# Kernel tuning notes

Measured on AMD Instinct MI355X. Metric: run time of the kernel, lower is better.

The kernel has to match this reference:

```python
import jax, jax.numpy as jnp
import numpy as np

B, C, H, W = 4, 128, 64, 64

def setup_inputs() -> dict:
    key = jax.random.key(0)
    ks = jax.random.split(key, 4)
    X = jax.random.normal(ks[0], (B, C, H, W), dtype=jnp.float32)
    Wq = jax.random.normal(ks[1], (C, C), dtype=jnp.float32) * 0.05
    Wk = jax.random.normal(ks[2], (C, C), dtype=jnp.float32) * 0.05
    Wv = jax.random.normal(ks[3], (C, C), dtype=jnp.float32) * 0.05
    bq = jnp.zeros((C,), dtype=jnp.float32)
    bk = jnp.zeros((C,), dtype=jnp.float32)
    bv = jnp.zeros((C,), dtype=jnp.float32)
    return {"X": X, "Wq": Wq, "bq": bq, "Wk": Wk, "bk": bk, "Wv": Wv, "bv": bv}

def reference(X, Wq, bq, Wk, bk, Wv, bv):
    b, c, h, w = X.shape
    hw = h * w
    # 1x1 conv == per-pixel linear over channels
    def proj(Wm, bias):
        y = jnp.einsum('bchw,oc->bohw', X, Wm) + bias[None, :, None, None]
        return y.reshape(b, c, hw).transpose(0, 2, 1)  # (b, hw, c)
    q = proj(Wq, bq)
    k = proj(Wk, bk)
    v = proj(Wv, bv)
    scores = jnp.einsum('bic,bjc->bij', q, k)  # (b, hw_q, hw_k); no 1/sqrt(d)
    # torch Softmax(dim=1) on (b, hw, hw): normalize over the QUERY axis
    a = jax.nn.softmax(scores, axis=1)
    x = jnp.einsum('bij,bjc->bic', a, v)  # (b, hw, c)
    x = x.transpose(0, 2, 1).reshape(b, c, h, w)
    return X + x
```

## Files before the change

### kernel.cpp

```cpp
#include <hip/hip_runtime.h>
#include <hip/hip_bf16.h>


typedef unsigned short u16;
typedef __attribute__((ext_vector_type(8))) __bf16 bf16x8;
typedef __attribute__((ext_vector_type(8))) unsigned short us8;
typedef __attribute__((ext_vector_type(4))) float f32x4;
typedef __attribute__((ext_vector_type(16))) float f32x16;

#define NB 4
#define CH 128
#define NP 4096
#define JSPL 4
#define ISPL 8

__device__ __forceinline__ float bf2f(u16 b){ union{float f;unsigned u;}v; v.u=((unsigned)b)<<16; return v.f; }
__device__ __forceinline__ u16 f2bf(float f){ union{float f;unsigned u;}v; v.f=f; unsigned r=v.u + 0x7FFFu + ((v.u>>16)&1u); return (u16)(r>>16); }

__device__ __forceinline__ f32x4 mfma16(bf16x8 a, bf16x8 b, f32x4 c){
  return __builtin_amdgcn_mfma_f32_16x16x32_bf16(a, b, c, 0, 0, 0);
}
__device__ __forceinline__ f32x16 mfma32(bf16x8 a, bf16x8 b, f32x16 c){
  return __builtin_amdgcn_mfma_f32_32x32x16_bf16(a, b, c, 0, 0, 0);
}
__device__ __forceinline__ bf16x8 ld8(const u16* p){
  union { us8 u; bf16x8 b; } v; v.u = *(const us8*)p; return v.b;
}
__device__ __forceinline__ void split8(const float* p, bf16x8& h, bf16x8& l){
  union { us8 u; bf16x8 b; } uh, ul;
  #pragma unroll
  for (int e=0;e<8;++e){
    float f = p[e];
    u16 hb = f2bf(f);
    uh.u[e] = hb;
    ul.u[e] = f2bf(f - bf2f(hb));
  }
  h = uh.b; l = ul.b;
}
__device__ __forceinline__ unsigned pk2(float a, float b){
  float2 f2; f2.x = a; f2.y = b;
  __hip_bfloat162 hb = __float22bfloat162_rn(f2);
  unsigned u; __builtin_memcpy(&u, &hb, 4);
  return u;
}
__device__ __forceinline__ void gll16(const void* g, void* l){
  __builtin_amdgcn_global_load_lds((const __attribute__((address_space(1))) void*)g,
                                   (__attribute__((address_space(3))) void*)l, 16, 0, 0);
}

__global__ __launch_bounds__(256) void wsplit_kernel(
    const float* __restrict__ Wq, const float* __restrict__ Wk,
    const float* __restrict__ Wv, u16* __restrict__ Whi, u16* __restrict__ Wlo)
{
  const int m = blockIdx.y;
  const float* W = (m==0) ? Wq : (m==1) ? Wk : Wv;
  int i = blockIdx.x*256 + threadIdx.x;
  float f = W[i];
  u16 hb = f2bf(f);
  Whi[m*CH*CH + i] = hb;
  Wlo[m*CH*CH + i] = f2bf(f - bf2f(hb));
}

__global__ __launch_bounds__(64) void proj_kernel(
    const float* __restrict__ X,
    const u16* __restrict__ Whi, const u16* __restrict__ Wlo,
    const float* __restrict__ bq, const float* __restrict__ bk,
    const float* __restrict__ bv,
    u16* __restrict__ Qhi, u16* __restrict__ Qlo,
    u16* __restrict__ Khi, u16* __restrict__ Klo,
    u16* __restrict__ Vthi, u16* __restrict__ Vtlo)
{
  __shared__ float XT[16][CH+4];
  const int b = blockIdx.y, p0 = blockIdx.x*16, lane = threadIdx.x;
  #pragma unroll
  for (int h=0; h<2; ++h){
    int c = lane + h*64;
    const float* src = X + ((size_t)b*CH + c)*NP + p0;
    #pragma unroll
    for (int v4=0; v4<4; ++v4){
      f32x4 v = *(const f32x4*)(src + v4*4);
      #pragma unroll
      for (int p=0;p<4;++p) XT[v4*4+p][c] = v[p];
    }
  }
  __syncthreads();
  const int l15 = lane&15, quad = lane>>4;
  bf16x8 xh[4], xl[4];
  #pragma unroll
  for (int s=0;s<4;++s) split8(&XT[l15][s*32+quad*8], xh[s], xl[s]);

  const float* bm[2] = {bq, bk};
  u16* OH[2] = {Qhi, Khi};
  u16* OL[2] = {Qlo, Klo};
  #pragma unroll
  for (int m=0;m<2;++m){
    const u16* WH = Whi + m*CH*CH;
    const u16* WL = Wlo + m*CH*CH;
    #pragma unroll
    for (int nt=0;nt<8;++nt){
      f32x4 a = {0.f,0.f,0.f,0.f};
      #pragma unroll
      for (int s=0;s<4;++s){
        size_t g = (size_t)(nt*16+l15)*CH + s*32 + quad*8;
        bf16x8 wh = ld8(&WH[g]), wl = ld8(&WL[g]);
        a = mfma16(xh[s], wl, a);
        a = mfma16(xl[s], wh, a);
        a = mfma16(xh[s], wh, a);
      }
      int o = nt*16 + l15;
      float bias = bm[m][o];
      #pragma unroll
      for (int r=0;r<4;++r){
        int i = p0 + quad*4 + r;
        float q = a[r] + bias;
        u16 hb = f2bf(q);
        size_t idx = ((size_t)b*NP + i)*CH + o;
        OH[m][idx] = hb;
        OL[m][idx] = f2bf(q - bf2f(hb));
      }
    }
  }
  const u16* WH = Whi + 2*CH*CH;
  const u16* WL = Wlo + 2*CH*CH;
  #pragma unroll
  for (int mt=0;mt<8;++mt){
    f32x4 a = {0.f,0.f,0.f,0.f};
    #pragma unroll
    for (int s=0;s<4;++s){
      size_t g = (size_t)(mt*16+l15)*CH + s*32 + quad*8;
      bf16x8 wh = ld8(&WH[g]), wl = ld8(&WL[g]);
      a = mfma16(wh, xl[s], a);
      a = mfma16(wl, xh[s], a);
      a = mfma16(wh, xh[s], a);
    }
    #pragma unroll
    for (int r=0;r<4;++r){
      int co = mt*16 + quad*4 + r;
      float v = a[r] + bv[co];
      u16 hb = f2bf(v);
      size_t idx = ((size_t)b*CH + co)*NP + p0 + l15;
      Vthi[idx] = hb;
      Vtlo[idx] = f2bf(v - bf2f(hb));
    }
  }
}

__global__ __launch_bounds__(256,3) void stats_kernel(
    const u16* __restrict__ Qhi, const u16* __restrict__ Qlo,
    const u16* __restrict__ Khi, const u16* __restrict__ Klo,
    float* __restrict__ colpart)
{
  __shared__ u16 SQ[2][2][32*CH];
  const int b = blockIdx.z, isplit = blockIdx.y;
  const int tid = threadIdx.x, lane = tid&63, w = tid>>6;
  const int l31 = lane&31, h = lane>>5;
  const int j0w = blockIdx.x*128 + w*32;

  const int slot0 = w*128 + lane, slot1 = slot0 + 64;
  const int qr0 = slot0&31, qc0 = slot0>>5, qr1 = slot1&31, qc1 = slot1>>5;
  const size_t qg0 = ((size_t)b*NP + qr0)*CH + qc0*8;
  const size_t qg1 = ((size_t)b*NP + qr1)*CH + qc1*8;
  const int lof0 = slot0*8, lof1 = slot1*8;

  bf16x8 kh[8], kl[8];
  #pragma unroll
  for (int ks=0;ks<8;++ks){
    size_t g = ((size_t)b*NP + j0w + l31)*CH + ks*16 + h*8;
    kh[ks] = ld8(&Khi[g]);
    kl[ks] = ld8(&Klo[g]);
  }

  const int ibase = isplit*(NP/ISPL);
  const int NCH = (NP/ISPL)/32;

  auto stageQ = [&](int t){
    size_t iofs = (size_t)(ibase + t*32)*CH;
    int bf = t&1;
    gll16(&Qhi[qg0 + iofs], &SQ[bf][0][lof0]);
    gll16(&Qhi[qg1 + iofs], &SQ[bf][0][lof1]);
    gll16(&Qlo[qg0 + iofs], &SQ[bf][1][lof0]);
    gll16(&Qlo[qg1 + iofs], &SQ[bf][1][lof1]);
  };
  auto computeS = [&](int t, f32x16& s){
    const u16* Qh = &SQ[t&1][0][0];
    const u16* Ql = &SQ[t&1][1][0];
    #pragma unroll
    for (int r=0;r<16;++r) s[r] = 0.f;
    #pragma unroll
    for (int ks=0;ks<8;++ks){
      int o = (ks*2+h)*256 + l31*8;
      bf16x8 qbh = ld8(&Qh[o]);
      bf16x8 qbl = ld8(&Ql[o]);
      s = mfma32(kh[ks], qbl, s);
      s = mfma32(kl[ks], qbh, s);
      s = mfma32(kh[ks], qbh, s);
    }
  };

  stageQ(0); stageQ(1);
  __syncthreads();
  f32x16 s;
  computeS(0, s);
  __syncthreads();

  float scol[16];
  #pragma unroll
  for (int r=0;r<16;++r) scol[r] = 0.f;

  for (int ic=0; ic<NCH; ++ic){
    if (ic+2 < NCH) stageQ(ic+2);
    #pragma unroll
    for (int r=0;r<16;++r) scol[r] += __expf(s[r]);
    if (ic+1 < NCH) computeS(ic+1, s);
    __syncthreads();
  }
  #pragma unroll
  for (int m=1; m<32; m<<=1){
    #pragma unroll
    for (int r=0;r<16;++r) scol[r] += __shfl_xor(scol[r], m);
  }
  if (l31 == 0){
    #pragma unroll
    for (int r=0;r<16;++r){
      int j = j0w + (r&3) + 8*(r>>2) + 4*h;
      colpart[((size_t)(isplit*NB + b))*NP + j] = scol[r];
    }
  }
}

__global__ __launch_bounds__(256) void scalev_kernel(
    u16* __restrict__ Vthi, const u16* __restrict__ Vtlo,
    const float* __restrict__ colpart)
{
  size_t t = (size_t)blockIdx.x*256 + threadIdx.x;
  size_t base = t*8;
  int bc = (int)(base >> 12);
  int b  = bc >> 7;
  int j0 = (int)(base & (NP-1));
  f32x4 s0 = {0.f,0.f,0.f,0.f}, s1 = {0.f,0.f,0.f,0.f};
  #pragma unroll
  for (int k=0;k<ISPL;++k){
    const float* cp = &colpart[((size_t)(k*NB + b))*NP + j0];
    f32x4 a0 = *(const f32x4*)cp;
    f32x4 a1 = *(const f32x4*)(cp+4);
    #pragma unroll
    for (int e=0;e<4;++e){ s0[e]+=a0[e]; s1[e]+=a1[e]; }
  }
  us8 hh = *(const us8*)&Vthi[base];
  us8 ll = *(const us8*)&Vtlo[base];
  us8 oh;
  #pragma unroll
  for (int e=0;e<8;++e){
    float r = 1.0f / (e<4 ? s0[e] : s1[e-4]);
    float v = (bf2f(hh[e]) + bf2f(ll[e])) * r;
    oh[e] = f2bf(v);
  }
  *(us8*)&Vthi[base] = oh;
}

__global__ __launch_bounds__(256) void copyx_kernel(
    const float* __restrict__ X, float* __restrict__ out)
{
  size_t idx = ((size_t)blockIdx.x*256 + threadIdx.x)*4;
  *(f32x4*)&out[idx] = *(const f32x4*)&X[idx];
}

__global__ __launch_bounds__(256,2) void attn_kernel(
    const u16* __restrict__ Qhi, const u16* __restrict__ Qlo,
    const u16* __restrict__ Khi, const u16* __restrict__ Klo,
    const u16* __restrict__ Vthi,
    float* __restrict__ out)
{
  __shared__ u16 SK[2][2][32*CH];
  __shared__ u16 SV[2][4*CH*8];
  const int b = blockIdx.z, jsplit = blockIdx.y;
  const int tid = threadIdx.x, lane = tid&63, w = tid>>6;
  const int l31 = lane&31, h = lane>>5;
  const int i0w = blockIdx.x*128 + w*32;
  const bool hb1 = (h != 0);

  const int slot0 = tid, slot1 = tid + 256;
  const int kr0 = slot0&31, kc0 = slot0>>5, kr1 = slot1&31, kc1 = slot1>>5;
  const int vr0 = slot0&127, vc0 = slot0>>7, vr1 = slot1&127, vc1 = slot1>>7;
  const size_t kg0 = ((size_t)b*NP + kr0)*CH + kc0*8;
  const size_t kg1 = ((size_t)b*NP + kr1)*CH + kc1*8;
  const size_t vg0 = ((size_t)b*CH + vr0)*NP + vc0*8;
  const size_t vg1 = ((size_t)b*CH + vr1)*NP + vc1*8;
  const int lof0 = slot0*8, lof1 = slot1*8;

  const int jbase = jsplit*(NP/JSPL);
  const int NJT = (NP/JSPL)/32;

  auto stageK = [&](int t){
    size_t jofs = (size_t)(jbase + t*32)*CH;
    int bf = t&1;
    gll16(&Khi[kg0 + jofs], &SK[bf][0][lof0]);
    gll16(&Khi[kg1 + jofs], &SK[bf][0][lof1]);
    gll16(&Klo[kg0 + jofs], &SK[bf][1][lof0]);
    gll16(&Klo[kg1 + jofs], &SK[bf][1][lof1]);
  };
  auto stageV = [&](int t){
    int j0 = jbase + t*32;
    int bf = t&1;
    gll16(&Vthi[vg0 + j0], &SV[bf][lof0]);
    gll16(&Vthi[vg1 + j0], &SV[bf][lof1]);
  };

  bf16x8 qh[8], ql[8];
  #pragma unroll
  for (int ks=0;ks<8;++ks){
    size_t g = ((size_t)b*NP + i0w + l31)*CH + ks*16 + h*8;
    qh[ks] = ld8(&Qhi[g]); ql[ks] = ld8(&Qlo[g]);
  }

  auto computeS = [&](int t, f32x16& s){
    const u16* Kh = &SK[t&1][0][0];
    const u16* Kl = &SK[t&1][1][0];
    #pragma unroll
    for (int r=0;r<16;++r) s[r] = 0.f;
    #pragma unroll
    for (int ks=0;ks<8;++ks){
      int o = (ks*2+h)*256 + l31*8;
      bf16x8 ah = ld8(&Kh[o]);
      bf16x8 al = ld8(&Kl[o]);
      s = mfma32(ah, ql[ks], s);
      s = mfma32(al, qh[ks], s);
      s = mfma32(ah, qh[ks], s);
    }
  };

  f32x16 acc[4];
  #pragma unroll
  for (int mt=0;mt<4;++mt)
    #pragma unroll
    for (int r=0;r<16;++r) acc[mt][r] = 0.f;

  stageK(0); stageV(0); stageK(1);
  __syncthreads();
  f32x16 s;
  computeS(0, s);
  __syncthreads();

  for (int jt=0; jt<NJT; ++jt){
    const int cb = jt&1;
    if (jt+2 < NJT) stageK(jt+2);
    if (jt+1 < NJT) stageV(jt+1);

    float p[16];
    #pragma unroll
    for (int r=0;r<16;++r) p[r] = __expf(s[r]);

    if (jt+1 < NJT) computeS(jt+1, s);

    const u16* Vh = &SV[cb][0];
    #pragma unroll
    for (int t=0;t<2;++t){
      unsigned hA = pk2(p[8*t+0], p[8*t+1]);
      unsigned hB = pk2(p[8*t+2], p[8*t+3]);
      unsigned hC = pk2(p[8*t+4], p[8*t+5]);
      unsigned hD = pk2(p[8*t+6], p[8*t+7]);
      unsigned s0h = hb1? hA:hC, s1h = hb1? hB:hD;
      unsigned r0h = __shfl_xor(s0h, 32), r1h = __shfl_xor(s1h, 32);
      unsigned dh[4];
      dh[0] = hb1? r0h : hA;  dh[1] = hb1? r1h : hB;
      dh[2] = hb1? hC  : r0h; dh[3] = hb1? hD  : r1h;
      bf16x8 Bh;
      __builtin_memcpy(&Bh, dh, 16);
      #pragma unroll
      for (int mt=0;mt<4;++mt){
        int o = (t*2+h)*1024 + (mt*32+l31)*8;
        bf16x8 vh = ld8(&Vh[o]);
        acc[mt] = mfma32(vh, Bh, acc[mt]);
      }
    }
    __syncthreads();
  }
  float* xp = out + (size_t)b*CH*NP;
  #pragma unroll
  for (int mt=0;mt<4;++mt){
    #pragma unroll
    for (int r=0;r<16;++r){
      int c = mt*32 + (r&3) + 8*(r>>2) + 4*h;
      atomicAdd(&xp[(size_t)c*NP + i0w + l31], acc[mt][r]);
    }
  }
}

extern "C" void kernel_launch(void* const* d_in, const int* in_sizes, int n_in,
                              void* d_out, int out_size, void* d_ws, size_t ws_size,
                              hipStream_t stream)
{
  const float* X  = (const float*)d_in[0];
  const float* Wq = (const float*)d_in[1];
  const float* bq = (const float*)d_in[2];
  const float* Wk = (const float*)d_in[3];
  const float* bk = (const float*)d_in[4];
  const float* Wv = (const float*)d_in[5];
  const float* bv = (const float*)d_in[6];
  float* outp = (float*)d_out;

  const size_t n = (size_t)NB*NP*CH;
  u16* Qhi = (u16*)d_ws;
  u16* Qlo = Qhi + n;
  u16* Khi = Qlo + n;
  u16* Klo = Khi + n;
  u16* Vthi = Klo + n;
  u16* Vtlo = Vthi + n;
  u16* Whi  = Vtlo + n;
  u16* Wlo  = Whi + 3*CH*CH;
  float* colpart = (float*)(Wlo + 3*CH*CH);

  wsplit_kernel<<<dim3(CH*CH/256, 3),      256, 0, stream>>>(Wq, Wk, Wv, Whi, Wlo);
  proj_kernel  <<<dim3(NP/16, NB),          64, 0, stream>>>(X, Whi, Wlo, bq, bk, bv,
                                                             Qhi,Qlo, Khi,Klo, Vthi,Vtlo);
  stats_kernel <<<dim3(NP/128, ISPL, NB),  256, 0, stream>>>(Qhi,Qlo, Khi,Klo, colpart);
  scalev_kernel<<<dim3(n/(256*8)),         256, 0, stream>>>(Vthi, Vtlo, colpart);
  copyx_kernel <<<dim3(n/(256*4)),         256, 0, stream>>>(X, outp);
  attn_kernel  <<<dim3(NP/128, JSPL, NB),  256, 0, stream>>>(Qhi,Qlo, Khi,Klo,
                                                             Vthi, outp);
}
```

Before: 254.4 us.

## Materialize exp scores in stats pass and reuse them in attention

The stats kernel now writes the bf16 exp(S) matrix, already packed in MFMA fragment order, to a workspace buffer. A new attention kernel then streams P and V from memory instead of recomputing QK^T with three split-precision MFMAs per tile. This trades the second score computation for writing and reading a 4x4096x4096 bf16 buffer (about 128 MB each way). The new path runs only if the workspace is large enough; otherwise the old fused path is used.

After: 250.2 us. Within noise of the previous version (-1.7%).

```diff
diff --git a/kernel.cpp b/kernel.cpp
--- a/kernel.cpp
+++ b/kernel.cpp
@@ -11,8 +11,9 @@
 #define NB 4
 #define CH 128
 #define NP 4096
-#define JSPL 4
 #define ISPL 8
+#define JSPLF 4
+#define JSPLP 8
 
 __device__ __forceinline__ float bf2f(u16 b){ union{float f;unsigned u;}v; v.u=((unsigned)b)<<16; return v.f; }
 __device__ __forceinline__ u16 f2bf(float f){ union{float f;unsigned u;}v; v.f=f; unsigned r=v.u + 0x7FFFu + ((v.u>>16)&1u); return (u16)(r>>16); }
@@ -42,6 +43,18 @@
   __hip_bfloat162 hb = __float22bfloat162_rn(f2);
   unsigned u; __builtin_memcpy(&u, &hb, 4);
   return u;
+}
+__device__ __forceinline__ us8 pfrag(const float* p, bool hb1){
+  unsigned hA = pk2(p[0], p[1]);
+  unsigned hB = pk2(p[2], p[3]);
+  unsigned hC = pk2(p[4], p[5]);
+  unsigned hD = pk2(p[6], p[7]);
+  unsigned s0h = hb1? hA:hC, s1h = hb1? hB:hD;
+  unsigned r0h = __shfl_xor(s0h, 32), r1h = __shfl_xor(s1h, 32);
+  unsigned dh[4];
+  dh[0] = hb1? r0h : hA;  dh[1] = hb1? r1h : hB;
+  dh[2] = hb1? hC  : r0h; dh[3] = hb1? hD  : r1h;
+  us8 o; __builtin_memcpy(&o, dh, 16); return o;
 }
 __device__ __forceinline__ void gll16(const void* g, void* l){
   __builtin_amdgcn_global_load_lds((const __attribute__((address_space(1))) void*)g,
@@ -145,16 +158,18 @@
   }
 }
 
+template<bool STOREP>
 __global__ __launch_bounds__(256,3) void stats_kernel(
     const u16* __restrict__ Qhi, const u16* __restrict__ Qlo,
     const u16* __restrict__ Khi, const u16* __restrict__ Klo,
-    float* __restrict__ colpart)
+    float* __restrict__ colpart, u16* __restrict__ Pbuf)
 {
   __shared__ u16 SQ[2][2][32*CH];
   const int b = blockIdx.z, isplit = blockIdx.y;
   const int tid = threadIdx.x, lane = tid&63, w = tid>>6;
   const int l31 = lane&31, h = lane>>5;
   const int j0w = blockIdx.x*128 + w*32;
+  const bool hb1 = (h != 0);
 
   const int slot0 = w*128 + lane, slot1 = slot0 + 64;
   const int qr0 = slot0&31, qc0 = slot0>>5, qr1 = slot1&31, qc1 = slot1>>5;
@@ -172,6 +187,7 @@
 
   const int ibase = isplit*(NP/ISPL);
   const int NCH = (NP/ISPL)/32;
+  const size_t Pjt = ((size_t)(b*128 + blockIdx.x*4 + w))*((size_t)4*NP*8);
 
   auto stageQ = [&](int t){
     size_t iofs = (size_t)(ibase + t*32)*CH;
@@ -209,8 +225,17 @@
 
   for (int ic=0; ic<NCH; ++ic){
     if (ic+2 < NCH) stageQ(ic+2);
-    #pragma unroll
-    for (int r=0;r<16;++r) scol[r] += __expf(s[r]);
+    float p[16];
+    #pragma unroll
+    for (int r=0;r<16;++r){ p[r] = __expf(s[r]); scol[r] += p[r]; }
+    if (STOREP){
+      int iglob = ibase + ic*32 + l31;
+      #pragma unroll
+      for (int t=0;t<2;++t){
+        us8 frag = pfrag(&p[8*t], hb1);
+        *(us8*)&Pbuf[Pjt + ((size_t)((t*2+h)*NP) + iglob)*8] = frag;
+      }
+    }
     if (ic+1 < NCH) computeS(ic+1, s);
     __syncthreads();
   }
@@ -265,7 +290,72 @@
   *(f32x4*)&out[idx] = *(const f32x4*)&X[idx];
 }
 
-__global__ __launch_bounds__(256,2) void attn_kernel(
+__global__ __launch_bounds__(256,4) void attnp_kernel(
+    const u16* __restrict__ Pbuf, const u16* __restrict__ Vthi,
+    float* __restrict__ out)
+{
+  __shared__ u16 SP[2][4*128*8];
+  __shared__ u16 SV[2][4*CH*8];
+  const int b = blockIdx.z, jsplit = blockIdx.y;
+  const int tid = threadIdx.x, lane = tid&63, w = tid>>6;
+  const int l31 = lane&31, h = lane>>5;
+  const int i0blk = blockIdx.x*128;
+  const int i0w = i0blk + w*32;
+
+  const int slot1 = tid + 256;
+  const size_t vg0 = ((size_t)b*CH + (tid  &127))*NP + (tid  >>7)*8;
+  const size_t vg1 = ((size_t)b*CH + (slot1&127))*NP + (slot1>>7)*8;
+  const size_t pg0 = (size_t)((tid  >>7)*NP) + i0blk + (tid  &127);
+  const size_t pg1 = (size_t)((slot1>>7)*NP) + i0blk + (slot1&127);
+
+  const int NJT = (NP/JSPLP)/32;
+
+  auto stage = [&](int t){
+    int bf = t&1;
+    size_t Pjt = ((size_t)(b*128 + jsplit*NJT + t))*((size_t)4*NP*8);
+    gll16(&Pbuf[Pjt + pg0*8], &SP[bf][tid*8]);
+    gll16(&Pbuf[Pjt + pg1*8], &SP[bf][slot1*8]);
+    int j0 = jsplit*(NP/JSPLP) + t*32;
+    gll16(&Vthi[vg0 + j0], &SV[bf][tid*8]);
+    gll16(&Vthi[vg1 + j0], &SV[bf][slot1*8]);
+  };
+
+  f32x16 acc[4];
+  #pragma unroll
+  for (int mt=0;mt<4;++mt)
+    #pragma unroll
+    for (int r=0;r<16;++r) acc[mt][r] = 0.f;
+
+  stage(0);
+  __syncthreads();
+
+  for (int jt=0; jt<NJT; ++jt){
+    const int cb = jt&1;
+    if (jt+1 < NJT) stage(jt+1);
+    #pragma unroll
+    for (int t=0;t<2;++t){
+      bf16x8 Bh = ld8(&SP[cb][((t*2+h)*128 + w*32 + l31)*8]);
+      #pragma unroll
+      for (int mt=0;mt<4;++mt){
+        int o = (t*2+h)*1024 + (mt*32+l31)*8;
+        bf16x8 vh = ld8(&SV[cb][o]);
+        acc[mt] = mfma32(vh, Bh, acc[mt]);
+      }
+    }
+    __syncthreads();
+  }
+  float* xp = out + (size_t)b*CH*NP;
+  #pragma unroll
+  for (int mt=0;mt<4;++mt){
+    #pragma unroll
+    for (int r=0;r<16;++r){
+      int c = mt*32 + (r&3) + 8*(r>>2) + 4*h;
+      atomicAdd(&xp[(size_t)c*NP + i0w + l31], acc[mt][r]);
+    }
+  }
+}
+
+__global__ __launch_bounds__(256,2) void attnf_kernel(
     const u16* __restrict__ Qhi, const u16* __restrict__ Qlo,
     const u16* __restrict__ Khi, const u16* __restrict__ Klo,
     const u16* __restrict__ Vthi,
@@ -281,15 +371,14 @@
 
   const int slot0 = tid, slot1 = tid + 256;
   const int kr0 = slot0&31, kc0 = slot0>>5, kr1 = slot1&31, kc1 = slot1>>5;
-  const int vr0 = slot0&127, vc0 = slot0>>7, vr1 = slot1&127, vc1 = slot1>>7;
   const size_t kg0 = ((size_t)b*NP + kr0)*CH + kc0*8;
   const size_t kg1 = ((size_t)b*NP + kr1)*CH + kc1*8;
-  const size_t vg0 = ((size_t)b*CH + vr0)*NP + vc0*8;
-  const size_t vg1 = ((size_t)b*CH + vr1)*NP + vc1*8;
+  const size_t vg0 = ((size_t)b*CH + (slot0&127))*NP + (slot0>>7)*8;
+  const size_t vg1 = ((size_t)b*CH + (slot1&127))*NP + (slot1>>7)*8;
   const int lof0 = slot0*8, lof1 = slot1*8;
 
-  const int jbase = jsplit*(NP/JSPL);
-  const int NJT = (NP/JSPL)/32;
+  const int jbase = jsplit*(NP/JSPLF);
+  const int NJT = (NP/JSPLF)/32;
 
   auto stageK = [&](int t){
     size_t jofs = (size_t)(jbase + t*32)*CH;
@@ -355,17 +444,8 @@
     const u16* Vh = &SV[cb][0];
     #pragma unroll
     for (int t=0;t<2;++t){
-      unsigned hA = pk2(p[8*t+0], p[8*t+1]);
-      unsigned hB = pk2(p[8*t+2], p[8*t+3]);
-      unsigned hC = pk2(p[8*t+4], p[8*t+5]);
-      unsigned hD = pk2(p[8*t+6], p[8*t+7]);
-      unsigned s0h = hb1? hA:hC, s1h = hb1? hB:hD;
-      unsigned r0h = __shfl_xor(s0h, 32), r1h = __shfl_xor(s1h, 32);
-      unsigned dh[4];
-      dh[0] = hb1? r0h : hA;  dh[1] = hb1? r1h : hB;
-      dh[2] = hb1? hC  : r0h; dh[3] = hb1? hD  : r1h;
-      bf16x8 Bh;
-      __builtin_memcpy(&Bh, dh, 16);
+      us8 fr = pfrag(&p[8*t], hb1);
+      bf16x8 Bh; __builtin_memcpy(&Bh, &fr, 16);
       #pragma unroll
       for (int mt=0;mt<4;++mt){
         int o = (t*2+h)*1024 + (mt*32+l31)*8;
@@ -409,13 +489,27 @@
   u16* Whi  = Vtlo + n;
   u16* Wlo  = Whi + 3*CH*CH;
   float* colpart = (float*)(Wlo + 3*CH*CH);
+  u16* Pbuf = (u16*)(colpart + (size_t)ISPL*NB*NP);
+
+  const size_t pelems = (size_t)NB*128*4*NP*8;
+  const size_t need = (size_t)((char*)Pbuf - (char*)d_ws) + pelems*sizeof(u16);
+  const bool usep = (ws_size >= need);
 
   wsplit_kernel<<<dim3(CH*CH/256, 3),      256, 0, stream>>>(Wq, Wk, Wv, Whi, Wlo);
   proj_kernel  <<<dim3(NP/16, NB),          64, 0, stream>>>(X, Whi, Wlo, bq, bk, bv,
                                                              Qhi,Qlo, Khi,Klo, Vthi,Vtlo);
-  stats_kernel <<<dim3(NP/128, ISPL, NB),  256, 0, stream>>>(Qhi,Qlo, Khi,Klo, colpart);
-  scalev_kernel<<<dim3(n/(256*8)),         256, 0, stream>>>(Vthi, Vtlo, colpart);
-  copyx_kernel <<<dim3(n/(256*4)),         256, 0, stream>>>(X, outp);
-  attn_kernel  <<<dim3(NP/128, JSPL, NB),  256, 0, stream>>>(Qhi,Qlo, Khi,Klo,
-                                                             Vthi, outp);
-}
+  if (usep){
+    stats_kernel<true><<<dim3(NP/128, ISPL, NB), 256, 0, stream>>>(
+        Qhi,Qlo, Khi,Klo, colpart, Pbuf);
+    scalev_kernel<<<dim3(n/(256*8)),       256, 0, stream>>>(Vthi, Vtlo, colpart);
+    copyx_kernel <<<dim3(n/(256*4)),       256, 0, stream>>>(X, outp);
+    attnp_kernel <<<dim3(NP/128, JSPLP, NB), 256, 0, stream>>>(Pbuf, Vthi, outp);
+  } else {
+    stats_kernel<false><<<dim3(NP/128, ISPL, NB), 256, 0, stream>>>(
+        Qhi,Qlo, Khi,Klo, colpart, Pbuf);
+    scalev_kernel<<<dim3(n/(256*8)),       256, 0, stream>>>(Vthi, Vtlo, colpart);
+    copyx_kernel <<<dim3(n/(256*4)),       256, 0, stream>>>(X, outp);
+    attnf_kernel <<<dim3(NP/128, JSPLF, NB), 256, 0, stream>>>(
+        Qhi,Qlo, Khi,Klo, Vthi, outp);
+  }
+}
```
